# Kernel tuning notes

Measured on AMD Instinct MI355X. Metric: run time of the kernel, lower is better.

The kernel has to match this reference:

```python
import jax, jax.numpy as jnp
import numpy as np

B, T, D = 4096, 200, 64
H0, H1 = 128, 64
NEG = float(-2**32 + 1)  # tf padding value


def setup_inputs() -> dict:
    key = jax.random.key(0)
    ks = jax.random.split(key, 8)
    q = jax.random.normal(ks[0], (B, D), dtype=jnp.float32)
    k = jax.random.normal(ks[1], (B, T, D), dtype=jnp.float32)
    v = jax.random.normal(ks[2], (B, T, D), dtype=jnp.float32)
    mask = jax.random.randint(ks[3], (B, T), 0, 2).astype(jnp.int32)
    W0 = jax.random.normal(ks[4], (4 * D, H0), dtype=jnp.float32) * (1.0 / np.sqrt(4 * D))
    b0 = jnp.zeros((H0,), dtype=jnp.float32)
    W1 = jax.random.normal(ks[5], (H0, H1), dtype=jnp.float32) * (1.0 / np.sqrt(H0))
    b1 = jnp.zeros((H1,), dtype=jnp.float32)
    Wf = jax.random.normal(ks[6], (H1, 1), dtype=jnp.float32) * (1.0 / np.sqrt(H1))
    bf = jnp.zeros((1,), dtype=jnp.float32)
    return {"q": q, "k": k, "v": v, "mask": mask,
            "W0": W0, "b0": b0, "W1": W1, "b1": b1, "Wf": Wf, "bf": bf}


def reference(q, k, v, mask, W0, b0, W1, b1, Wf, bf):
    # tile q across history positions: [B, D] -> [B, T, D]
    qt = jnp.broadcast_to(q[:, None, :], k.shape)
    # DIN interaction features: [B, T, 4D]
    info = jnp.concatenate([qt, k, qt - k, qt * k], axis=-1)
    # small scorer MLP (Dense+relu, Dense+relu, Dense(1))
    h = jax.nn.relu(jnp.einsum('btf,fh->bth', info, W0) + b0)
    h = jax.nn.relu(jnp.einsum('btf,fh->bth', h, W1) + b1)
    logits = (jnp.einsum('btf,fh->bth', h, Wf) + bf)[..., 0]  # [B, T]
    # mask then softmax over history
    logits = jnp.where(mask == 0, NEG, logits)
    att = jax.nn.softmax(logits, axis=-1)  # [B, T]
    # weighted pooling: [B, T] x [B, T, D] -> [B, D]
    return jnp.einsum('bt,btd->bd', att, v)
```

## Files before the change

kernel.cpp:

```cpp
#include <hip/hip_runtime.h>

typedef __attribute__((ext_vector_type(4))) _Float16 f16x4;
typedef __attribute__((ext_vector_type(8))) _Float16 f16x8;
typedef __attribute__((ext_vector_type(4))) float f32x4;

#define NB 4096
#define TT 200
#define DD 64
#define H0 128
#define H1 64

#define WS_BC 0
#define WS_DD 16384
#define WS_W1 32768
#define WS_CB 49152

__global__ __launch_bounds__(256)
void pre_fold(const float* __restrict__ W0, const float* __restrict__ W1,
              unsigned char* __restrict__ ws)
{
  int idx = blockIdx.x * 256 + threadIdx.x;
  _Float16* bcT  = (_Float16*)(ws + WS_BC);
  _Float16* ddT  = (_Float16*)(ws + WS_DD);
  _Float16* w1p  = (_Float16*)(ws + WS_W1);
  if (idx < 8192) {
    int h = idx >> 6, d = idx & 63;
    bcT[h * 64 + d] = (_Float16)(W0[(64 + d) * H0 + h] - W0[(128 + d) * H0 + h]);
    ddT[h * 64 + d] = (_Float16)(W0[(192 + d) * H0 + h]);
  } else {
    int i = idx - 8192;
    int jrow = i >> 7, p = i & 127;
    int m = p >> 5, g4p = (p >> 3) & 3, jj = p & 7;
    int h = 32 * m + 16 * (jj >> 2) + 4 * g4p + (jj & 3);
    int up = p >> 3, wi = p & 7;
    w1p[jrow * 128 + (((up ^ (jrow & 15)) << 3) | wi)] = (_Float16)W1[h * H1 + jrow];
  }
}

__global__ __launch_bounds__(256)
void pre_cb(const float* __restrict__ q, const float* __restrict__ W0,
            const float* __restrict__ b0, unsigned char* __restrict__ ws)
{
  __shared__ float WacS[DD * H0];
  __shared__ float qS2[2][DD];
  const int tid = threadIdx.x;
  float* cb = (float*)(ws + WS_CB);

  #pragma unroll 4
  for (int i = 0; i < 32; ++i) {
    int idx = i * 256 + tid;
    int d = idx >> 7, h = idx & 127;
    WacS[idx] = W0[d * H0 + h] + W0[(128 + d) * H0 + h];
  }
  __syncthreads();

  const int half = tid >> 7, h = tid & 127;
  #pragma unroll 1
  for (int p = 0; p < 16; ++p) {
    int bpair = blockIdx.x * 32 + p * 2;
    if (tid < DD) qS2[0][tid] = q[(size_t)bpair * DD + tid];
    else if (tid >= 128 && tid < 128 + DD) qS2[1][tid - 128] = q[(size_t)(bpair + 1) * DD + (tid - 128)];
    __syncthreads();
    float s = b0[h];
    #pragma unroll 8
    for (int d = 0; d < DD; ++d) s = fmaf(qS2[half][d], WacS[d * H0 + h], s);
    cb[(size_t)(bpair + half) * H0 + h] = s;
    __syncthreads();
  }
}

__global__ __launch_bounds__(256, 4)
void din_attn(const float* __restrict__ q, const float* __restrict__ k,
              const float* __restrict__ v, const int* __restrict__ mask,
              const float* __restrict__ b1, const float* __restrict__ Wf,
              const unsigned char* __restrict__ ws, float* __restrict__ out)
{
  const int b    = blockIdx.x;
  const int tid  = threadIdx.x;
  const int lane = tid & 63;
  const int wid  = tid >> 6;
  const int r16  = lane & 15;
  const int g4   = lane >> 4;

  __shared__ __align__(16) _Float16 MhT[H0 * 64];
  __shared__ __align__(16) _Float16 W1p[H1 * 128];
  __shared__ float qS[DD];
  __shared__ float cbS[H0];
  __shared__ float b1S[H1];
  __shared__ float WfS[H1];
  __shared__ float sP[208];
  __shared__ float red[8];
  __shared__ float pool[256];

  const float* qb = q + b * DD;
  const float* kb = k + (size_t)b * TT * DD;
  const float* vb = v + (size_t)b * TT * DD;
  const int*   mb = mask + b * TT;

  {
    const uint4* src = (const uint4*)(ws + WS_W1);
    uint4* dst = (uint4*)W1p;
    #pragma unroll
    for (int i = 0; i < 4; ++i) dst[i * 256 + tid] = src[i * 256 + tid];
  }
  if (tid < DD) qS[tid] = qb[tid];
  if (tid < H0) cbS[tid] = ((const float*)(ws + WS_CB))[(size_t)b * H0 + tid];
  if (tid >= H0 && tid < H0 + H1) b1S[tid - H0] = b1[tid - H0];
  if (tid >= H0 + H1 && tid < H0 + 2 * H1) WfS[tid - H0 - H1] = Wf[tid - H0 - H1];
  __syncthreads();

  {
    const _Float16* bcT = (const _Float16*)(ws + WS_BC);
    const _Float16* ddT = (const _Float16*)(ws + WS_DD);
    const int u    = tid & 7;
    const int dblk = u * 8;
    const int h4 = (tid >> 3) * 4;
    float q8[8];
    #pragma unroll
    for (int j = 0; j < 8; ++j) q8[j] = qS[dblk + j];
    #pragma unroll
    for (int hi = 0; hi < 4; ++hi) {
      const int h = h4 + hi;
      f16x8 bc8 = *(const f16x8*)(bcT + h * 64 + dblk);
      f16x8 dd8 = *(const f16x8*)(ddT + h * 64 + dblk);
      f16x8 o8;
      #pragma unroll
      for (int j = 0; j < 8; ++j)
        o8[j] = (_Float16)((float)bc8[j] + q8[j] * (float)dd8[j]);
      *(f16x8*)(&MhT[h * 64 + ((u ^ (h & 7)) << 3)]) = o8;
    }
  }

  const int dof = 8 * g4;
  float4 kq[4];
  {
    const int trow = wid * 16 + r16;
    kq[0] = *(const float4*)(kb + trow * DD + dof);
    kq[1] = *(const float4*)(kb + trow * DD + dof + 4);
    kq[2] = *(const float4*)(kb + trow * DD + 32 + dof);
    kq[3] = *(const float4*)(kb + trow * DD + 32 + dof + 4);
  }
  __syncthreads();

  const int k8 = r16 & 7;
  const int kW = r16;

  #pragma unroll 1
  for (int s = wid; s < 13; s += 4) {
    const int t0   = s * 16;
    const int trow = t0 + r16;
    int mm = (trow < TT) ? mb[trow] : -1;

    f16x8 bh0, bh1;
    {
      float f0[8] = {kq[0].x, kq[0].y, kq[0].z, kq[0].w,
                     kq[1].x, kq[1].y, kq[1].z, kq[1].w};
      float f1[8] = {kq[2].x, kq[2].y, kq[2].z, kq[2].w,
                     kq[3].x, kq[3].y, kq[3].z, kq[3].w};
      #pragma unroll
      for (int j = 0; j < 8; ++j) {
        bh0[j] = (_Float16)f0[j];
        bh1[j] = (_Float16)f1[j];
      }
    }
    const int sn = s + 4;
    if (sn < 13) {
      const int trn = sn * 16 + r16;
      if (trn < TT) {
        kq[0] = *(const float4*)(kb + trn * DD + dof);
        kq[1] = *(const float4*)(kb + trn * DD + dof + 4);
        kq[2] = *(const float4*)(kb + trn * DD + 32 + dof);
        kq[3] = *(const float4*)(kb + trn * DD + 32 + dof + 4);
      } else {
        float4 z = {0.f, 0.f, 0.f, 0.f};
        kq[0] = z; kq[1] = z; kq[2] = z; kq[3] = z;
      }
    }

    f32x4 acc1[4];
    #pragma unroll
    for (int c1 = 0; c1 < 4; ++c1) acc1[c1] = (f32x4){0.f, 0.f, 0.f, 0.f};

    #pragma unroll 1
    for (int m = 0; m < 4; ++m) {
      const _Float16* rowE = &MhT[((2 * m) * 16 + r16) * 64];
      const _Float16* rowO = rowE + 16 * 64;
      f16x8 afE0 = *(const f16x8*)(rowE + ((g4 ^ k8) << 3));
      f16x8 afE1 = *(const f16x8*)(rowE + (((g4 + 4) ^ k8) << 3));
      f32x4 a0e = {0.f, 0.f, 0.f, 0.f};
      a0e = __builtin_amdgcn_mfma_f32_16x16x32_f16(afE0, bh0, a0e, 0, 0, 0);
      a0e = __builtin_amdgcn_mfma_f32_16x16x32_f16(afE1, bh1, a0e, 0, 0, 0);
      f16x8 afO0 = *(const f16x8*)(rowO + ((g4 ^ k8) << 3));
      f16x8 afO1 = *(const f16x8*)(rowO + (((g4 + 4) ^ k8) << 3));
      f32x4 a0o = {0.f, 0.f, 0.f, 0.f};
      a0o = __builtin_amdgcn_mfma_f32_16x16x32_f16(afO0, bh0, a0o, 0, 0, 0);
      a0o = __builtin_amdgcn_mfma_f32_16x16x32_f16(afO1, bh1, a0o, 0, 0, 0);

      f32x4 cbe = *(const f32x4*)(&cbS[(2 * m) * 16 + 4 * g4]);
      f32x4 cbo = *(const f32x4*)(&cbS[(2 * m) * 16 + 16 + 4 * g4]);
      f16x8 hf;
      #pragma unroll
      for (int r = 0; r < 4; ++r) {
        float he = a0e[r] + cbe[r];
        float ho = a0o[r] + cbo[r];
        hf[r]     = (_Float16)(he > 0.f ? he : 0.f);
        hf[4 + r] = (_Float16)(ho > 0.f ? ho : 0.f);
      }
      #pragma unroll
      for (int c1 = 0; c1 < 4; ++c1) {
        f16x8 af1 = *(const f16x8*)(&W1p[(c1 * 16 + r16) * 128
                                         + (((4 * m + g4) ^ kW) << 3)]);
        acc1[c1] = __builtin_amdgcn_mfma_f32_16x16x32_f16(af1, hf, acc1[c1], 0, 0, 0);
      }
    }

    float p = 0.f;
    #pragma unroll
    for (int c1 = 0; c1 < 4; ++c1) {
      f32x4 b14 = *(const f32x4*)(&b1S[c1 * 16 + 4 * g4]);
      f32x4 wf4 = *(const f32x4*)(&WfS[c1 * 16 + 4 * g4]);
      #pragma unroll
      for (int r = 0; r < 4; ++r) {
        float h1 = acc1[c1][r] + b14[r];
        h1 = h1 > 0.f ? h1 : 0.f;
        p = fmaf(h1, wf4[r], p);
      }
    }

    p += __shfl_xor(p, 16, 64);
    p += __shfl_xor(p, 32, 64);
    p = (mm == 1) ? p : (mm == 0 ? -1e30f : -2e30f);
    if (g4 == 0) sP[t0 + r16] = p;
  }
  __syncthreads();

  const int tg = lane >> 4;
  const int dq = lane & 15;
  const int tbase = wid * 52;
  f32x4 vv[13];
  #pragma unroll
  for (int i = 0; i < 13; ++i) {
    int t = tbase + i * 4 + tg;
    int tc = t < TT ? t : TT - 1;
    vv[i] = *(const f32x4*)(vb + tc * DD + dq * 4);
  }

  float rcpS;
  {
    float val = (tid < 208) ? sP[tid] : -3e30f;
    float mx = val;
    #pragma unroll
    for (int off = 32; off >= 1; off >>= 1) mx = fmaxf(mx, __shfl_xor(mx, off, 64));
    if (lane == 0) red[wid] = mx;
    __syncthreads();
    float M = fmaxf(fmaxf(red[0], red[1]), fmaxf(red[2], red[3]));
    float e = (tid < 208) ? __expf(val - M) : 0.f;
    float se = e;
    #pragma unroll
    for (int off = 32; off >= 1; off >>= 1) se += __shfl_xor(se, off, 64);
    if (lane == 0) red[4 + wid] = se;
    __syncthreads();
    rcpS = 1.f / ((red[4] + red[5]) + (red[6] + red[7]));
    if (tid < 208) sP[tid] = e;
  }
  __syncthreads();

  {
    f32x4 o4 = {0.f, 0.f, 0.f, 0.f};
    #pragma unroll
    for (int i = 0; i < 13; ++i) {
      int t = tbase + i * 4 + tg;
      float w = (t < TT) ? sP[t] : 0.f;
      #pragma unroll
      for (int j = 0; j < 4; ++j) o4[j] = fmaf(w, vv[i][j], o4[j]);
    }
    #pragma unroll
    for (int j = 0; j < 4; ++j) {
      o4[j] += __shfl_xor(o4[j], 16, 64);
      o4[j] += __shfl_xor(o4[j], 32, 64);
    }
    if (tg == 0) *(f32x4*)(&pool[wid * 64 + dq * 4]) = o4;
  }
  __syncthreads();

  if (tid < DD)
    out[b * DD + tid] = ((pool[tid] + pool[64 + tid])
                       + (pool[128 + tid] + pool[192 + tid])) * rcpS;
}

extern "C" void kernel_launch(void* const* d_in, const int* in_sizes, int n_in,
                              void* d_out, int out_size, void* d_ws, size_t ws_size,
                              hipStream_t stream) {
  const float* q    = (const float*)d_in[0];
  const float* k    = (const float*)d_in[1];
  const float* v    = (const float*)d_in[2];
  const int*   mask = (const int*)d_in[3];
  const float* W0   = (const float*)d_in[4];
  const float* b0   = (const float*)d_in[5];
  const float* W1   = (const float*)d_in[6];
  const float* b1   = (const float*)d_in[7];
  const float* Wf   = (const float*)d_in[8];
  float* out = (float*)d_out;
  unsigned char* ws = (unsigned char*)d_ws;

  pre_fold<<<dim3(64), dim3(256), 0, stream>>>(W0, W1, ws);
  pre_cb<<<dim3(128), dim3(256), 0, stream>>>(q, W0, b0, ws);
  din_attn<<<dim3(NB), dim3(256), 0, stream>>>(q, k, v, mask, b1, Wf, ws, out);
}
```

Measured before the change: 122.0 us.

## Widen attention block to 13 waves so each wave scores one tile

The attention kernel now launches 832 threads per batch row (13 wavefronts) instead of 256. Each wave handles exactly one 16-row history tile, which removes the strided tile loop and the manual K-prefetch. Shared-memory setup, the MhT build, the V pooling and the softmax reductions are redistributed over the wider block, with 13-way reductions. The aim is more waves in flight per CU, since shared-memory use per block stays about the same, so latency from the serial per-wave loop is hidden better. The cost is larger barrier groups, and a launch-bounds hint that may constrain registers.

```diff
diff --git a/kernel.cpp b/kernel.cpp
--- a/kernel.cpp
+++ b/kernel.cpp
@@ -9,6 +9,7 @@
 #define DD 64
 #define H0 128
 #define H1 64
+#define BT 832
 
 #define WS_BC 0
 #define WS_DD 16384
@@ -69,7 +70,7 @@
   }
 }
 
-__global__ __launch_bounds__(256, 4)
+__global__ __launch_bounds__(BT, 6)
 void din_attn(const float* __restrict__ q, const float* __restrict__ k,
               const float* __restrict__ v, const int* __restrict__ mask,
               const float* __restrict__ b1, const float* __restrict__ Wf,
@@ -84,13 +85,13 @@
 
   __shared__ __align__(16) _Float16 MhT[H0 * 64];
   __shared__ __align__(16) _Float16 W1p[H1 * 128];
-  __shared__ float qS[DD];
-  __shared__ float cbS[H0];
-  __shared__ float b1S[H1];
-  __shared__ float WfS[H1];
+  __shared__ __align__(16) float qS[DD];
+  __shared__ __align__(16) float cbS[H0];
+  __shared__ __align__(16) float b1S[H1];
+  __shared__ __align__(16) float WfS[H1];
   __shared__ float sP[208];
-  __shared__ float red[8];
-  __shared__ float pool[256];
+  __shared__ float red[32];
+  __shared__ float pool[13 * 64];
 
   const float* qb = q + b * DD;
   const float* kb = k + (size_t)b * TT * DD;
@@ -100,80 +101,54 @@
   {
     const uint4* src = (const uint4*)(ws + WS_W1);
     uint4* dst = (uint4*)W1p;
-    #pragma unroll
-    for (int i = 0; i < 4; ++i) dst[i * 256 + tid] = src[i * 256 + tid];
+    dst[tid < 1024 ? tid : 0] = src[tid < 1024 ? tid : 0];
+    if (tid < 192) dst[832 + tid] = src[832 + tid];
   }
   if (tid < DD) qS[tid] = qb[tid];
-  if (tid < H0) cbS[tid] = ((const float*)(ws + WS_CB))[(size_t)b * H0 + tid];
-  if (tid >= H0 && tid < H0 + H1) b1S[tid - H0] = b1[tid - H0];
-  if (tid >= H0 + H1 && tid < H0 + 2 * H1) WfS[tid - H0 - H1] = Wf[tid - H0 - H1];
-  __syncthreads();
-
-  {
+  else if (tid >= 64 && tid < 64 + H0)
+    cbS[tid - 64] = ((const float*)(ws + WS_CB))[(size_t)b * H0 + (tid - 64)];
+  else if (tid >= 192 && tid < 192 + H1) b1S[tid - 192] = b1[tid - 192];
+  else if (tid >= 256 && tid < 256 + H1) WfS[tid - 256] = Wf[tid - 256];
+
+  const int dof = 8 * g4;
+  const int t0   = wid * 16;
+  const int trow = t0 + r16;
+  const int tck  = trow < TT ? trow : TT - 1;
+  float4 kq0 = *(const float4*)(kb + tck * DD + dof);
+  float4 kq1 = *(const float4*)(kb + tck * DD + dof + 4);
+  float4 kq2 = *(const float4*)(kb + tck * DD + 32 + dof);
+  float4 kq3 = *(const float4*)(kb + tck * DD + 32 + dof + 4);
+  const int mm = (trow < TT) ? mb[trow] : -1;
+  __syncthreads();
+
+  #pragma unroll 1
+  for (int idx = tid; idx < 1024; idx += BT) {
     const _Float16* bcT = (const _Float16*)(ws + WS_BC);
     const _Float16* ddT = (const _Float16*)(ws + WS_DD);
-    const int u    = tid & 7;
+    const int u = idx & 7, h = idx >> 3;
     const int dblk = u * 8;
-    const int h4 = (tid >> 3) * 4;
-    float q8[8];
-    #pragma unroll
-    for (int j = 0; j < 8; ++j) q8[j] = qS[dblk + j];
-    #pragma unroll
-    for (int hi = 0; hi < 4; ++hi) {
-      const int h = h4 + hi;
-      f16x8 bc8 = *(const f16x8*)(bcT + h * 64 + dblk);
-      f16x8 dd8 = *(const f16x8*)(ddT + h * 64 + dblk);
-      f16x8 o8;
-      #pragma unroll
-      for (int j = 0; j < 8; ++j)
-        o8[j] = (_Float16)((float)bc8[j] + q8[j] * (float)dd8[j]);
-      *(f16x8*)(&MhT[h * 64 + ((u ^ (h & 7)) << 3)]) = o8;
-    }
-  }
-
-  const int dof = 8 * g4;
-  float4 kq[4];
-  {
-    const int trow = wid * 16 + r16;
-    kq[0] = *(const float4*)(kb + trow * DD + dof);
-    kq[1] = *(const float4*)(kb + trow * DD + dof + 4);
-    kq[2] = *(const float4*)(kb + trow * DD + 32 + dof);
-    kq[3] = *(const float4*)(kb + trow * DD + 32 + dof + 4);
+    f16x8 bc8 = *(const f16x8*)(bcT + h * 64 + dblk);
+    f16x8 dd8 = *(const f16x8*)(ddT + h * 64 + dblk);
+    f16x8 o8;
+    #pragma unroll
+    for (int j = 0; j < 8; ++j)
+      o8[j] = (_Float16)((float)bc8[j] + qS[dblk + j] * (float)dd8[j]);
+    *(f16x8*)(&MhT[h * 64 + ((u ^ (h & 7)) << 3)]) = o8;
   }
   __syncthreads();
 
   const int k8 = r16 & 7;
   const int kW = r16;
 
-  #pragma unroll 1
-  for (int s = wid; s < 13; s += 4) {
-    const int t0   = s * 16;
-    const int trow = t0 + r16;
-    int mm = (trow < TT) ? mb[trow] : -1;
-
+  {
     f16x8 bh0, bh1;
     {
-      float f0[8] = {kq[0].x, kq[0].y, kq[0].z, kq[0].w,
-                     kq[1].x, kq[1].y, kq[1].z, kq[1].w};
-      float f1[8] = {kq[2].x, kq[2].y, kq[2].z, kq[2].w,
-                     kq[3].x, kq[3].y, kq[3].z, kq[3].w};
+      float f0[8] = {kq0.x, kq0.y, kq0.z, kq0.w, kq1.x, kq1.y, kq1.z, kq1.w};
+      float f1[8] = {kq2.x, kq2.y, kq2.z, kq2.w, kq3.x, kq3.y, kq3.z, kq3.w};
       #pragma unroll
       for (int j = 0; j < 8; ++j) {
         bh0[j] = (_Float16)f0[j];
         bh1[j] = (_Float16)f1[j];
-      }
-    }
-    const int sn = s + 4;
-    if (sn < 13) {
-      const int trn = sn * 16 + r16;
-      if (trn < TT) {
-        kq[0] = *(const float4*)(kb + trn * DD + dof);
-        kq[1] = *(const float4*)(kb + trn * DD + dof + 4);
-        kq[2] = *(const float4*)(kb + trn * DD + 32 + dof);
-        kq[3] = *(const float4*)(kb + trn * DD + 32 + dof + 4);
-      } else {
-        float4 z = {0.f, 0.f, 0.f, 0.f};
-        kq[0] = z; kq[1] = z; kq[2] = z; kq[3] = z;
       }
     }
 
@@ -226,7 +201,6 @@
         p = fmaf(h1, wf4[r], p);
       }
     }
-
     p += __shfl_xor(p, 16, 64);
     p += __shfl_xor(p, 32, 64);
     p = (mm == 1) ? p : (mm == 0 ? -1e30f : -2e30f);
@@ -236,13 +210,14 @@
 
   const int tg = lane >> 4;
   const int dq = lane & 15;
-  const int tbase = wid * 52;
-  f32x4 vv[13];
-  #pragma unroll
-  for (int i = 0; i < 13; ++i) {
-    int t = tbase + i * 4 + tg;
-    int tc = t < TT ? t : TT - 1;
-    vv[i] = *(const f32x4*)(vb + tc * DD + dq * 4);
+  f32x4 vv0, vv1, vv2, vv3;
+  {
+    int ta = t0 + 4 * 0 + tg, tb = t0 + 4 * 1 + tg;
+    int tc2 = t0 + 4 * 2 + tg, td = t0 + 4 * 3 + tg;
+    vv0 = *(const f32x4*)(vb + (ta < TT ? ta : TT - 1) * DD + dq * 4);
+    vv1 = *(const f32x4*)(vb + (tb < TT ? tb : TT - 1) * DD + dq * 4);
+    vv2 = *(const f32x4*)(vb + (tc2 < TT ? tc2 : TT - 1) * DD + dq * 4);
+    vv3 = *(const f32x4*)(vb + (td < TT ? td : TT - 1) * DD + dq * 4);
   }
 
   float rcpS;
@@ -253,27 +228,32 @@
     for (int off = 32; off >= 1; off >>= 1) mx = fmaxf(mx, __shfl_xor(mx, off, 64));
     if (lane == 0) red[wid] = mx;
     __syncthreads();
-    float M = fmaxf(fmaxf(red[0], red[1]), fmaxf(red[2], red[3]));
+    float M = red[0];
+    #pragma unroll
+    for (int w = 1; w < 13; ++w) M = fmaxf(M, red[w]);
     float e = (tid < 208) ? __expf(val - M) : 0.f;
     float se = e;
     #pragma unroll
     for (int off = 32; off >= 1; off >>= 1) se += __shfl_xor(se, off, 64);
-    if (lane == 0) red[4 + wid] = se;
-    __syncthreads();
-    rcpS = 1.f / ((red[4] + red[5]) + (red[6] + red[7]));
+    if (lane == 0) red[16 + wid] = se;
+    __syncthreads();
+    float S = 0.f;
+    #pragma unroll
+    for (int w = 0; w < 13; ++w) S += red[16 + w];
+    rcpS = 1.f / S;
     if (tid < 208) sP[tid] = e;
   }
   __syncthreads();
 
   {
     f32x4 o4 = {0.f, 0.f, 0.f, 0.f};
-    #pragma unroll
-    for (int i = 0; i < 13; ++i) {
-      int t = tbase + i * 4 + tg;
-      float w = (t < TT) ? sP[t] : 0.f;
-      #pragma unroll
-      for (int j = 0; j < 4; ++j) o4[j] = fmaf(w, vv[i][j], o4[j]);
-    }
+    float w0 = sP[t0 + 4 * 0 + tg];
+    float w1 = sP[t0 + 4 * 1 + tg];
+    float w2 = sP[t0 + 4 * 2 + tg];
+    float w3 = sP[t0 + 4 * 3 + tg];
+    #pragma unroll
+    for (int j = 0; j < 4; ++j)
+      o4[j] = fmaf(w0, vv0[j], fmaf(w1, vv1[j], fmaf(w2, vv2[j], w3 * vv3[j])));
     #pragma unroll
     for (int j = 0; j < 4; ++j) {
       o4[j] += __shfl_xor(o4[j], 16, 64);
@@ -283,9 +263,12 @@
   }
   __syncthreads();
 
-  if (tid < DD)
-    out[b * DD + tid] = ((pool[tid] + pool[64 + tid])
-                       + (pool[128 + tid] + pool[192 + tid])) * rcpS;
+  if (tid < DD) {
+    float acc = 0.f;
+    #pragma unroll
+    for (int w = 0; w < 13; ++w) acc += pool[w * 64 + tid];
+    out[b * DD + tid] = acc * rcpS;
+  }
 }
 
 extern "C" void kernel_launch(void* const* d_in, const int* in_sizes, int n_in,
@@ -305,5 +288,5 @@
 
   pre_fold<<<dim3(64), dim3(256), 0, stream>>>(W0, W1, ws);
   pre_cb<<<dim3(128), dim3(256), 0, stream>>>(q, W0, b0, ws);
-  din_attn<<<dim3(NB), dim3(256), 0, stream>>>(q, k, v, mask, b1, Wf, ws, out);
-}
+  din_attn<<<dim3(NB), dim3(BT), 0, stream>>>(q, k, v, mask, b1, Wf, ws, out);
+}
```

New measurement: 154.2 us. 1.26x slower.

## Process two batch rows per 512-thread block sharing W1 staging

Applied to the files above, without the earlier changes.

Each block now handles two batch rows with 512 threads, so the W1 copy into shared memory is paid once per pair, and launch bounds rise to allow 6 blocks per CU. The k prefetch moves ahead of the first barrier so its global loads overlap the W1/q/cb staging. The pool buffer now reuses the per-row MhT space instead of its own array. Block-wide barriers now couple two independent rows, and the stricter launch bound may cause register spills.

```diff
diff --git a/kernel.cpp b/kernel.cpp
--- a/kernel.cpp
+++ b/kernel.cpp
@@ -9,6 +9,7 @@
 #define DD 64
 #define H0 128
 #define H1 64
+#define BT 512
 
 #define WS_BC 0
 #define WS_DD 16384
@@ -69,55 +70,68 @@
   }
 }
 
-__global__ __launch_bounds__(256, 4)
+__global__ __launch_bounds__(BT, 6)
 void din_attn(const float* __restrict__ q, const float* __restrict__ k,
               const float* __restrict__ v, const int* __restrict__ mask,
               const float* __restrict__ b1, const float* __restrict__ Wf,
               const unsigned char* __restrict__ ws, float* __restrict__ out)
 {
-  const int b    = blockIdx.x;
   const int tid  = threadIdx.x;
+  const int bloc = tid >> 8;
+  const int t256 = tid & 255;
   const int lane = tid & 63;
-  const int wid  = tid >> 6;
+  const int wid4 = (tid >> 6) & 3;
   const int r16  = lane & 15;
   const int g4   = lane >> 4;
-
-  __shared__ __align__(16) _Float16 MhT[H0 * 64];
+  const int b    = blockIdx.x * 2 + bloc;
+
   __shared__ __align__(16) _Float16 W1p[H1 * 128];
-  __shared__ float qS[DD];
-  __shared__ float cbS[H0];
-  __shared__ float b1S[H1];
-  __shared__ float WfS[H1];
-  __shared__ float sP[208];
-  __shared__ float red[8];
-  __shared__ float pool[256];
-
-  const float* qb = q + b * DD;
+  __shared__ __align__(16) _Float16 MhT2[2][H0 * 64];
+  __shared__ __align__(16) float qS[2][DD];
+  __shared__ __align__(16) float cbS[2][H0];
+  __shared__ __align__(16) float b1S[H1];
+  __shared__ __align__(16) float WfS[H1];
+  __shared__ float sP[2][208];
+  __shared__ float red[2][8];
+
+  const float* qb = q + (size_t)b * DD;
   const float* kb = k + (size_t)b * TT * DD;
   const float* vb = v + (size_t)b * TT * DD;
-  const int*   mb = mask + b * TT;
+  const int*   mb = mask + (size_t)b * TT;
 
   {
     const uint4* src = (const uint4*)(ws + WS_W1);
     uint4* dst = (uint4*)W1p;
-    #pragma unroll
-    for (int i = 0; i < 4; ++i) dst[i * 256 + tid] = src[i * 256 + tid];
-  }
-  if (tid < DD) qS[tid] = qb[tid];
-  if (tid < H0) cbS[tid] = ((const float*)(ws + WS_CB))[(size_t)b * H0 + tid];
-  if (tid >= H0 && tid < H0 + H1) b1S[tid - H0] = b1[tid - H0];
-  if (tid >= H0 + H1 && tid < H0 + 2 * H1) WfS[tid - H0 - H1] = Wf[tid - H0 - H1];
+    dst[tid]       = src[tid];
+    dst[512 + tid] = src[512 + tid];
+  }
+  if (t256 < DD) qS[bloc][t256] = qb[t256];
+  else if (t256 >= 64 && t256 < 64 + H0)
+    cbS[bloc][t256 - 64] = ((const float*)(ws + WS_CB))[(size_t)b * H0 + (t256 - 64)];
+  if (tid >= 192 && tid < 192 + H1) b1S[tid - 192] = b1[tid - 192];
+  if (tid >= 448 && tid < 448 + H1) WfS[tid - 448] = Wf[tid - 448];
+
+  const int dof = 8 * g4;
+  float4 kq[4];
+  {
+    const int trow = wid4 * 16 + r16;
+    kq[0] = *(const float4*)(kb + trow * DD + dof);
+    kq[1] = *(const float4*)(kb + trow * DD + dof + 4);
+    kq[2] = *(const float4*)(kb + trow * DD + 32 + dof);
+    kq[3] = *(const float4*)(kb + trow * DD + 32 + dof + 4);
+  }
   __syncthreads();
 
   {
     const _Float16* bcT = (const _Float16*)(ws + WS_BC);
     const _Float16* ddT = (const _Float16*)(ws + WS_DD);
-    const int u    = tid & 7;
+    _Float16* Mh = MhT2[bloc];
+    const int u    = t256 & 7;
     const int dblk = u * 8;
-    const int h4 = (tid >> 3) * 4;
+    const int h4 = (t256 >> 3) * 4;
     float q8[8];
     #pragma unroll
-    for (int j = 0; j < 8; ++j) q8[j] = qS[dblk + j];
+    for (int j = 0; j < 8; ++j) q8[j] = qS[bloc][dblk + j];
     #pragma unroll
     for (int hi = 0; hi < 4; ++hi) {
       const int h = h4 + hi;
@@ -127,26 +141,17 @@
       #pragma unroll
       for (int j = 0; j < 8; ++j)
         o8[j] = (_Float16)((float)bc8[j] + q8[j] * (float)dd8[j]);
-      *(f16x8*)(&MhT[h * 64 + ((u ^ (h & 7)) << 3)]) = o8;
-    }
-  }
-
-  const int dof = 8 * g4;
-  float4 kq[4];
-  {
-    const int trow = wid * 16 + r16;
-    kq[0] = *(const float4*)(kb + trow * DD + dof);
-    kq[1] = *(const float4*)(kb + trow * DD + dof + 4);
-    kq[2] = *(const float4*)(kb + trow * DD + 32 + dof);
-    kq[3] = *(const float4*)(kb + trow * DD + 32 + dof + 4);
+      *(f16x8*)(&Mh[h * 64 + ((u ^ (h & 7)) << 3)]) = o8;
+    }
   }
   __syncthreads();
 
   const int k8 = r16 & 7;
   const int kW = r16;
+  const _Float16* Mh = MhT2[bloc];
 
   #pragma unroll 1
-  for (int s = wid; s < 13; s += 4) {
+  for (int s = wid4; s < 13; s += 4) {
     const int t0   = s * 16;
     const int trow = t0 + r16;
     int mm = (trow < TT) ? mb[trow] : -1;
@@ -183,7 +188,7 @@
 
     #pragma unroll 1
     for (int m = 0; m < 4; ++m) {
-      const _Float16* rowE = &MhT[((2 * m) * 16 + r16) * 64];
+      const _Float16* rowE = &Mh[((2 * m) * 16 + r16) * 64];
       const _Float16* rowO = rowE + 16 * 64;
       f16x8 afE0 = *(const f16x8*)(rowE + ((g4 ^ k8) << 3));
       f16x8 afE1 = *(const f16x8*)(rowE + (((g4 + 4) ^ k8) << 3));
@@ -196,8 +201,8 @@
       a0o = __builtin_amdgcn_mfma_f32_16x16x32_f16(afO0, bh0, a0o, 0, 0, 0);
       a0o = __builtin_amdgcn_mfma_f32_16x16x32_f16(afO1, bh1, a0o, 0, 0, 0);
 
-      f32x4 cbe = *(const f32x4*)(&cbS[(2 * m) * 16 + 4 * g4]);
-      f32x4 cbo = *(const f32x4*)(&cbS[(2 * m) * 16 + 16 + 4 * g4]);
+      f32x4 cbe = *(const f32x4*)(&cbS[bloc][(2 * m) * 16 + 4 * g4]);
+      f32x4 cbo = *(const f32x4*)(&cbS[bloc][(2 * m) * 16 + 16 + 4 * g4]);
       f16x8 hf;
       #pragma unroll
       for (int r = 0; r < 4; ++r) {
@@ -230,13 +235,13 @@
     p += __shfl_xor(p, 16, 64);
     p += __shfl_xor(p, 32, 64);
     p = (mm == 1) ? p : (mm == 0 ? -1e30f : -2e30f);
-    if (g4 == 0) sP[t0 + r16] = p;
+    if (g4 == 0) sP[bloc][t0 + r16] = p;
   }
   __syncthreads();
 
   const int tg = lane >> 4;
   const int dq = lane & 15;
-  const int tbase = wid * 52;
+  const int tbase = wid4 * 52;
   f32x4 vv[13];
   #pragma unroll
   for (int i = 0; i < 13; ++i) {
@@ -247,30 +252,32 @@
 
   float rcpS;
   {
-    float val = (tid < 208) ? sP[tid] : -3e30f;
+    float val = (t256 < 208) ? sP[bloc][t256] : -3e30f;
     float mx = val;
     #pragma unroll
     for (int off = 32; off >= 1; off >>= 1) mx = fmaxf(mx, __shfl_xor(mx, off, 64));
-    if (lane == 0) red[wid] = mx;
+    if (lane == 0) red[bloc][wid4] = mx;
     __syncthreads();
-    float M = fmaxf(fmaxf(red[0], red[1]), fmaxf(red[2], red[3]));
-    float e = (tid < 208) ? __expf(val - M) : 0.f;
+    float M = fmaxf(fmaxf(red[bloc][0], red[bloc][1]),
+                    fmaxf(red[bloc][2], red[bloc][3]));
+    float e = (t256 < 208) ? __expf(val - M) : 0.f;
     float se = e;
     #pragma unroll
     for (int off = 32; off >= 1; off >>= 1) se += __shfl_xor(se, off, 64);
-    if (lane == 0) red[4 + wid] = se;
+    if (lane == 0) red[bloc][4 + wid4] = se;
     __syncthreads();
-    rcpS = 1.f / ((red[4] + red[5]) + (red[6] + red[7]));
-    if (tid < 208) sP[tid] = e;
-  }
-  __syncthreads();
-
+    rcpS = 1.f / ((red[bloc][4] + red[bloc][5]) + (red[bloc][6] + red[bloc][7]));
+    if (t256 < 208) sP[bloc][t256] = e;
+  }
+  __syncthreads();
+
+  float* poolb = (float*)MhT2[bloc];
   {
     f32x4 o4 = {0.f, 0.f, 0.f, 0.f};
     #pragma unroll
     for (int i = 0; i < 13; ++i) {
       int t = tbase + i * 4 + tg;
-      float w = (t < TT) ? sP[t] : 0.f;
+      float w = (t < TT) ? sP[bloc][t] : 0.f;
       #pragma unroll
       for (int j = 0; j < 4; ++j) o4[j] = fmaf(w, vv[i][j], o4[j]);
     }
@@ -279,13 +286,13 @@
       o4[j] += __shfl_xor(o4[j], 16, 64);
       o4[j] += __shfl_xor(o4[j], 32, 64);
     }
-    if (tg == 0) *(f32x4*)(&pool[wid * 64 + dq * 4]) = o4;
-  }
-  __syncthreads();
-
-  if (tid < DD)
-    out[b * DD + tid] = ((pool[tid] + pool[64 + tid])
-                       + (pool[128 + tid] + pool[192 + tid])) * rcpS;
+    if (tg == 0) *(f32x4*)(&poolb[wid4 * 64 + dq * 4]) = o4;
+  }
+  __syncthreads();
+
+  if (t256 < DD)
+    out[(size_t)b * DD + t256] = ((poolb[t256] + poolb[64 + t256])
+                                + (poolb[128 + t256] + poolb[192 + t256])) * rcpS;
 }
 
 extern "C" void kernel_launch(void* const* d_in, const int* in_sizes, int n_in,
@@ -305,5 +312,5 @@
 
   pre_fold<<<dim3(64), dim3(256), 0, stream>>>(W0, W1, ws);
   pre_cb<<<dim3(128), dim3(256), 0, stream>>>(q, W0, b0, ws);
-  din_attn<<<dim3(NB), dim3(256), 0, stream>>>(q, k, v, mask, b1, Wf, ws, out);
+  din_attn<<<dim3(NB / 2), dim3(BT), 0, stream>>>(q, k, v, mask, b1, Wf, ws, out);
 }
```

Measured after the change: 226.8 us. 86.0% more time.
